# Kernel optimization log

Measured on AMD Instinct MI355X. Metric: run time of the kernel, lower is better.

Reference implementation:

```python
import jax, jax.numpy as jnp
import numpy as np

IN, H, OUT = 128, 256, 128
B, T = 256, 512
EPS = 1e-5


def gru_cell(x, h, w_ih, w_hh, b_ih, b_hh):
    # PyTorch GRUCell: gates ordered (r, z, n)
    gi = x @ w_ih.T + b_ih            # (B, 3H)
    gh = h @ w_hh.T + b_hh            # (B, 3H)
    gi_r, gi_z, gi_n = jnp.split(gi, 3, axis=-1)
    gh_r, gh_z, gh_n = jnp.split(gh, 3, axis=-1)
    r = jax.nn.sigmoid(gi_r + gh_r)
    z = jax.nn.sigmoid(gi_z + gh_z)
    n = jnp.tanh(gi_n + r * gh_n)
    return (1.0 - z) * n + z * h


def setup_inputs() -> dict:
    key = jax.random.key(0)
    ks = jax.random.split(key, 12)
    s_in = 1.0 / np.sqrt(H)
    u = lambda k, shp: jax.random.uniform(k, shp, jnp.float32, -s_in, s_in)
    return {
        "x": jax.random.normal(ks[0], (B, T, IN), jnp.float32),
        "w_ih1": u(ks[1], (3 * H, IN)),
        "w_hh1": u(ks[2], (3 * H, H)),
        "b_ih1": u(ks[3], (3 * H,)),
        "b_hh1": u(ks[4], (3 * H,)),
        "w_ih2": u(ks[5], (3 * H, H)),
        "w_hh2": u(ks[6], (3 * H, H)),
        "b_ih2": u(ks[7], (3 * H,)),
        "b_hh2": u(ks[8], (3 * H,)),
        "gamma": jnp.ones((H,), jnp.float32),
        "beta": jnp.zeros((H,), jnp.float32),
        "fc_w": u(ks[9], (OUT, H)),
        "fc_b": u(ks[10], (OUT,)),
    }


def reference(x, w_ih1, w_hh1, b_ih1, b_hh1, w_ih2, w_hh2, b_ih2, b_hh2,
              gamma, beta, fc_w, fc_b):
    batch = x.shape[0]
    h0 = (jnp.zeros((batch, H), x.dtype), jnp.zeros((batch, H), x.dtype))

    def step(carry, xt):
        h1, h2 = carry
        h1 = gru_cell(xt, h1, w_ih1, w_hh1, b_ih1, b_hh1)
        h2 = gru_cell(h1, h2, w_ih2, w_hh2, b_ih2, b_hh2)
        return (h1, h2), h2

    _, seq_hidden = jax.lax.scan(step, h0, jnp.swapaxes(x, 0, 1))  # (T, B, H)
    seq_hidden = jnp.swapaxes(seq_hidden, 0, 1)                    # (B, T, H)

    # SyncBatchNorm in training mode: batch statistics over (batch*time)
    flat = seq_hidden.reshape(-1, H)
    mean = flat.mean(axis=0)
    var = flat.var(axis=0)  # biased variance, as used for normalization
    normed = (flat - mean) * jax.lax.rsqrt(var + EPS) * gamma + beta

    # Hardtanh(-2, 2), temporal mean, linear projection
    act = jnp.clip(normed, -2.0, 2.0).reshape(batch, -1, H)
    summary = act.mean(axis=1)                                     # (B, H)
    return summary @ fc_w.T + fc_b
```

## Files before the change

### kernel.cpp

```cpp
#include <hip/hip_runtime.h>
#include <stdint.h>

#define TT 512
#define BB 256
#define HH 256
#define II 128
#define OUTD 128
#define EPSV 1e-5f

#define NCL 32
#define RPC 8
#define RD1 32
#define RD2 16
#define HPAD 264
#define SPIN_CAP (1 << 17)

#define P_M1 0
#define P_A  1
#define P_M2 2
#define P_B  3

#define OFF_PROG     0u
#define OFF_BNSUM    1024u
#define OFF_BNSQ     2048u
#define OFF_ZERO_END 3072u
#define OFF_GI1      65536u
#define GI_SLOT      16384u
#define GI1_BYTES    ((unsigned)NCL*RD1*GI_SLOT)
#define OFF_H1R      (OFF_GI1 + GI1_BYTES)
#define H1R_BYTES    ((unsigned)NCL*RD2*4096u)
#define OFF_GI2      (OFF_H1R + H1R_BYTES)
#define GI2_BYTES    ((unsigned)NCL*RD2*GI_SLOT)
#define OFF_H2SEQ    (OFF_GI2 + GI2_BYTES)

typedef short bf16x8 __attribute__((ext_vector_type(8)));
typedef float f32x4  __attribute__((ext_vector_type(4)));
typedef unsigned long long u64;

__device__ __forceinline__ short f2bf(float v) {
    unsigned u = __float_as_uint(v);
    u += 0x7fffu + ((u >> 16) & 1u);
    return (short)(u >> 16);
}
__device__ __forceinline__ float bf2f(short s) {
    return __uint_as_float(((unsigned)(unsigned short)s) << 16);
}
__device__ __forceinline__ float bf2f_lo(unsigned u) {
    return __uint_as_float(u << 16);
}
__device__ __forceinline__ float bf2f_hi(unsigned u) {
    return __uint_as_float(u & 0xffff0000u);
}
__device__ __forceinline__ unsigned pk2bf(float a, float b) {
    return (unsigned)(unsigned short)f2bf(a) | ((unsigned)(unsigned short)f2bf(b) << 16);
}
__device__ __forceinline__ bf16x8 ldfrag_f32(const float* __restrict__ p) {
    const float4* q = (const float4*)p;
    float4 a = q[0], b = q[1];
    bf16x8 f;
    f[0]=f2bf(a.x); f[1]=f2bf(a.y); f[2]=f2bf(a.z); f[3]=f2bf(a.w);
    f[4]=f2bf(b.x); f[5]=f2bf(b.y); f[6]=f2bf(b.z); f[7]=f2bf(b.w);
    return f;
}
__device__ __forceinline__ float sigm_f(float x) {
    float e = __expf(-x);
    return __builtin_amdgcn_rcpf(1.f + e);
}
__device__ __forceinline__ float tanh_f(float x) {
    float ax = fabsf(x);
    float e  = __expf(-2.f * ax);
    float t  = (1.f - e) * __builtin_amdgcn_rcpf(1.f + e);
    return copysignf(t, x);
}
__device__ __forceinline__ void poll_ge(const unsigned* p, int tgt) {
    if (tgt <= 0) return;
    int spins = 0;
    while ((int)__hip_atomic_load((unsigned*)p, __ATOMIC_RELAXED, __HIP_MEMORY_SCOPE_SYSTEM) < tgt) {
        __builtin_amdgcn_s_sleep(2);
        if (++spins > SPIN_CAP) break;
    }
    asm volatile("" ::: "memory");
}
__device__ __forceinline__ void poll2_ge(const unsigned* p1, int t1, const unsigned* p2, int t2) {
    int spins = 0;
    for (;;) {
        int a = (int)__hip_atomic_load((unsigned*)p1, __ATOMIC_RELAXED, __HIP_MEMORY_SCOPE_SYSTEM);
        int b = (int)__hip_atomic_load((unsigned*)p2, __ATOMIC_RELAXED, __HIP_MEMORY_SCOPE_SYSTEM);
        if (a >= t1 && b >= t2) break;
        __builtin_amdgcn_s_sleep(2);
        if (++spins > SPIN_CAP) break;
    }
    asm volatile("" ::: "memory");
}
__device__ __forceinline__ void post_prog(unsigned* p, int v) {
    __hip_atomic_store(p, (unsigned)v, __ATOMIC_RELAXED, __HIP_MEMORY_SCOPE_SYSTEM);
}
__device__ __forceinline__ unsigned ld_u32_coh(const unsigned* p) {
    return __hip_atomic_load((unsigned*)p, __ATOMIC_RELAXED, __HIP_MEMORY_SCOPE_SYSTEM);
}
__device__ __forceinline__ void st_u32_coh(unsigned* p, unsigned v) {
    __hip_atomic_store(p, v, __ATOMIC_RELAXED, __HIP_MEMORY_SCOPE_SYSTEM);
}
__device__ __forceinline__ u64 ld_u64_coh(const u64* p) {
    return __hip_atomic_load((u64*)p, __ATOMIC_RELAXED, __HIP_MEMORY_SCOPE_SYSTEM);
}
__device__ __forceinline__ void st_u64_coh(u64* p, u64 v) {
    __hip_atomic_store(p, v, __ATOMIC_RELAXED, __HIP_MEMORY_SCOPE_SYSTEM);
}
#define CFENCE() asm volatile("" ::: "memory")

__global__ void __launch_bounds__(512, 1)
gru_pipe(const float* __restrict__ x,
         const float* __restrict__ wih1, const float* __restrict__ whh1,
         const float* __restrict__ bih1, const float* __restrict__ bhh1,
         const float* __restrict__ wih2, const float* __restrict__ whh2,
         const float* __restrict__ bih2, const float* __restrict__ bhh2,
         char* __restrict__ ws)
{
    const int tid = threadIdx.x, wave = tid >> 6, lane = tid & 63;
    const int qd = lane >> 4, ln = lane & 15;
    const int stage = blockIdx.x & 3;
    const int cl    = blockIdx.x >> 2;
    const int grow0 = cl * RPC;

    unsigned* prog = (unsigned*)(ws + OFF_PROG) + cl * 4;
    short* h2seq = (short*)(ws + OFF_H2SEQ);

    __shared__ __align__(16) short hb[2][16][HPAD];
    {
        short* z = &hb[0][0][0];
        for (int i = tid; i < 2*16*HPAD; i += 512) z[i] = 0;
    }
    __syncthreads();

    if (stage == 0) {
        bf16x8 Wi[2][3][4]; f32x4 cinit[2][3];
        #pragma unroll
        for (int b2 = 0; b2 < 2; ++b2)
        #pragma unroll
        for (int g = 0; g < 3; ++g) {
            const int grow = g*256 + (wave*2 + b2)*16 + ln;
            #pragma unroll
            for (int kc = 0; kc < 4; ++kc)
                Wi[b2][g][kc] = ldfrag_f32(wih1 + grow*II + kc*32 + qd*8);
            float c0 = bih1[grow] + (g < 2 ? bhh1[grow] : 0.f);
            cinit[b2][g] = f32x4{c0, c0, c0, c0};
        }
        const float* xr = x + (size_t)(grow0 + (ln>>2)*2 + (ln&1)) * (TT*II) + qd*8;
        float4 xp[8];
        #pragma unroll
        for (int kc = 0; kc < 4; ++kc) {
            xp[2*kc]   = *(const float4*)(xr + kc*32);
            xp[2*kc+1] = *(const float4*)(xr + kc*32 + 4);
        }

        for (int t = 0; t < TT; ++t) {
            if (tid == 0 && t >= 2) post_prog(&prog[P_M1], t);
            if ((t & 7) == 0) poll_ge(&prog[P_A], t - 24);
            CFENCE();
            bf16x8 a[4];
            #pragma unroll
            for (int kc = 0; kc < 4; ++kc) {
                float4 u = xp[2*kc], v = xp[2*kc+1];
                bf16x8 f;
                f[0]=f2bf(u.x); f[1]=f2bf(u.y); f[2]=f2bf(u.z); f[3]=f2bf(u.w);
                f[4]=f2bf(v.x); f[5]=f2bf(v.y); f[6]=f2bf(v.z); f[7]=f2bf(v.w);
                a[kc] = f;
            }
            if (t + 1 < TT) {
                const float* xn = xr + (size_t)(t+1)*II;
                #pragma unroll
                for (int kc = 0; kc < 4; ++kc) {
                    xp[2*kc]   = *(const float4*)(xn + kc*32);
                    xp[2*kc+1] = *(const float4*)(xn + kc*32 + 4);
                }
            }
            CFENCE();
            f32x4 acc[2][3];
            #pragma unroll
            for (int b2 = 0; b2 < 2; ++b2)
            #pragma unroll
            for (int g = 0; g < 3; ++g) acc[b2][g] = cinit[b2][g];
            #pragma unroll
            for (int kc = 0; kc < 4; ++kc)
            #pragma unroll
            for (int b2 = 0; b2 < 2; ++b2)
            #pragma unroll
            for (int g = 0; g < 3; ++g)
                acc[b2][g] = __builtin_amdgcn_mfma_f32_16x16x32_bf16(a[kc], Wi[b2][g][kc], acc[b2][g], 0, 0, 0);
            CFENCE();
            char* slot = ws + OFF_GI1 + ((size_t)cl*RD1 + (t & (RD1-1)))*GI_SLOT;
            unsigned* rz = (unsigned*)slot;
            u64* nn = (u64*)(slot + 8192);
            #pragma unroll
            for (int b2 = 0; b2 < 2; ++b2) {
                const int tile = wave*2 + b2;
                st_u32_coh(rz + (tile*2 + 0)*64 + lane, pk2bf(acc[b2][0][0], acc[b2][0][1]));
                st_u32_coh(rz + (tile*2 + 1)*64 + lane, pk2bf(acc[b2][1][0], acc[b2][1][1]));
                union { float f[2]; u64 u; } np;
                np.f[0] = acc[b2][2][0]; np.f[1] = acc[b2][2][1];
                st_u64_coh(nn + tile*64 + lane, np.u);
            }
            asm volatile("s_waitcnt vmcnt(14)" ::: "memory");
            __builtin_amdgcn_sched_barrier(0);
            __builtin_amdgcn_s_barrier();
        }
        __syncthreads();
        if (tid == 0) post_prog(&prog[P_M1], 1000000);

    } else if (stage == 1) {
        bf16x8 Wh[2][3][8]; float bnn[2];
        #pragma unroll
        for (int b2 = 0; b2 < 2; ++b2) {
            const int colg = (wave*2 + b2)*16 + ln;
            #pragma unroll
            for (int g = 0; g < 3; ++g)
                #pragma unroll
                for (int kc = 0; kc < 8; ++kc)
                    Wh[b2][g][kc] = ldfrag_f32(whh1 + (g*256 + colg)*HH + kc*32 + qd*8);
            bnn[b2] = bhh1[512 + colg];
        }
        float hold[2][2] = {{0.f,0.f},{0.f,0.f}};
        unsigned pr0, pr1, pz0, pz1; u64 pn0, pn1;
        const int tile0 = wave*2, tile1 = wave*2 + 1;

        poll_ge(&prog[P_M1], 2);
        {
            char* slot = ws + OFF_GI1 + (size_t)cl*RD1*GI_SLOT;
            const unsigned* rz = (const unsigned*)slot;
            const u64* nn = (const u64*)(slot + 8192);
            pr0 = ld_u32_coh(rz + (tile0*2+0)*64 + lane);
            pz0 = ld_u32_coh(rz + (tile0*2+1)*64 + lane);
            pn0 = ld_u64_coh(nn + tile0*64 + lane);
            pr1 = ld_u32_coh(rz + (tile1*2+0)*64 + lane);
            pz1 = ld_u32_coh(rz + (tile1*2+1)*64 + lane);
            pn1 = ld_u64_coh(nn + tile1*64 + lane);
        }

        for (int t = 0; t < TT; ++t) {
            if (tid == 0 && t >= 2) post_prog(&prog[P_A], t);
            if ((t & 7) == 0) poll2_ge(&prog[P_M1], t + 10, &prog[P_M2], t - 9);
            CFENCE();
            f32x4 aR[2], aZ[2], aN[2]; float gn[2][2];
            aR[0] = f32x4{bf2f_lo(pr0), bf2f_hi(pr0), 0.f, 0.f};
            aZ[0] = f32x4{bf2f_lo(pz0), bf2f_hi(pz0), 0.f, 0.f};
            aR[1] = f32x4{bf2f_lo(pr1), bf2f_hi(pr1), 0.f, 0.f};
            aZ[1] = f32x4{bf2f_lo(pz1), bf2f_hi(pz1), 0.f, 0.f};
            { union { u64 u; float f[2]; } c; c.u = pn0; gn[0][0]=c.f[0]; gn[0][1]=c.f[1];
              c.u = pn1; gn[1][0]=c.f[0]; gn[1][1]=c.f[1]; }
            aN[0] = f32x4{bnn[0], bnn[0], 0.f, 0.f};
            aN[1] = f32x4{bnn[1], bnn[1], 0.f, 0.f};
            if (t + 1 < TT) {
                char* slot = ws + OFF_GI1 + ((size_t)cl*RD1 + ((t+1) & (RD1-1)))*GI_SLOT;
                const unsigned* rz = (const unsigned*)slot;
                const u64* nn = (const u64*)(slot + 8192);
                pr0 = ld_u32_coh(rz + (tile0*2+0)*64 + lane);
                pz0 = ld_u32_coh(rz + (tile0*2+1)*64 + lane);
                pn0 = ld_u64_coh(nn + tile0*64 + lane);
                pr1 = ld_u32_coh(rz + (tile1*2+0)*64 + lane);
                pz1 = ld_u32_coh(rz + (tile1*2+1)*64 + lane);
                pn1 = ld_u64_coh(nn + tile1*64 + lane);
            }
            CFENCE();
            const int rb = (t + 1) & 1, wb = t & 1;
            #pragma unroll
            for (int kc = 0; kc < 8; ++kc) {
                bf16x8 f = *(const bf16x8*)&hb[rb][ln][kc*32 + qd*8];
                aR[0] = __builtin_amdgcn_mfma_f32_16x16x32_bf16(f, Wh[0][0][kc], aR[0], 0,0,0);
                aR[1] = __builtin_amdgcn_mfma_f32_16x16x32_bf16(f, Wh[1][0][kc], aR[1], 0,0,0);
                aZ[0] = __builtin_amdgcn_mfma_f32_16x16x32_bf16(f, Wh[0][1][kc], aZ[0], 0,0,0);
                aZ[1] = __builtin_amdgcn_mfma_f32_16x16x32_bf16(f, Wh[1][1][kc], aZ[1], 0,0,0);
                aN[0] = __builtin_amdgcn_mfma_f32_16x16x32_bf16(f, Wh[0][2][kc], aN[0], 0,0,0);
                aN[1] = __builtin_amdgcn_mfma_f32_16x16x32_bf16(f, Wh[1][2][kc], aN[1], 0,0,0);
            }
            CFENCE();
            unsigned* h1slot = (unsigned*)(ws + OFF_H1R + ((size_t)cl*RD2 + (t & (RD2-1)))*4096u);
            #pragma unroll
            for (int b2 = 0; b2 < 2; ++b2) {
                const int colg = (wave*2 + b2)*16 + ln;
                unsigned pk = 0;
                #pragma unroll
                for (int r = 0; r < 2; ++r) {
                    float rg = sigm_f(aR[b2][r]);
                    float zg = sigm_f(aZ[b2][r]);
                    float ng = tanh_f(gn[b2][r] + rg * aN[b2][r]);
                    float h  = (1.f - zg)*ng + zg*hold[b2][r];
                    hold[b2][r] = h;
                    short hs = f2bf(h);
                    hb[wb][qd*4 + r][colg] = hs;
                    pk |= (unsigned)(unsigned short)hs << (16*r);
                }
                st_u32_coh(h1slot + colg*4 + qd, pk);
            }
            asm volatile("s_waitcnt vmcnt(8) lgkmcnt(0)" ::: "memory");
            __builtin_amdgcn_sched_barrier(0);
            __builtin_amdgcn_s_barrier();
        }
        __syncthreads();
        if (tid == 0) post_prog(&prog[P_A], 1000000);

    } else if (stage == 2) {
        bf16x8 Wi[2][3][8]; float c0s[2][3];
        #pragma unroll
        for (int b2 = 0; b2 < 2; ++b2)
        #pragma unroll
        for (int g = 0; g < 3; ++g) {
            const int grow = g*256 + (wave*2 + b2)*16 + ln;
            #pragma unroll
            for (int kc = 0; kc < 8; ++kc)
                Wi[b2][g][kc] = ldfrag_f32(wih2 + grow*HH + kc*32 + qd*8);
            c0s[b2][g] = bih2[grow] + (g < 2 ? bhh2[grow] : 0.f);
        }
        const int base = (tid & 1) * 8, pcol = tid >> 1;
        u64 vcur;

        poll_ge(&prog[P_A], 2);
        {
            const u64* h1s = (const u64*)(ws + OFF_H1R + (size_t)cl*RD2*4096u);
            u64 v = ld_u64_coh(h1s + tid);
            unsigned lo = (unsigned)v, hi = (unsigned)(v >> 32);
            hb[0][base + 0][pcol] = (short)lo;
            hb[0][base + 1][pcol] = (short)(lo >> 16);
            hb[0][base + 4][pcol] = (short)hi;
            hb[0][base + 5][pcol] = (short)(hi >> 16);
        }
        poll_ge(&prog[P_A], 3);
        vcur = ld_u64_coh((const u64*)(ws + OFF_H1R + ((size_t)cl*RD2 + 1)*4096u) + tid);
        __syncthreads();

        for (int u = 0; u < TT; ++u) {
            if (tid == 0 && u >= 2) post_prog(&prog[P_M2], u);
            if ((u & 1) == 0) poll2_ge(&prog[P_A], u + 5, &prog[P_B], u - 13);
            CFENCE();
            if (u + 1 < TT) {
                unsigned lo = (unsigned)vcur, hi = (unsigned)(vcur >> 32);
                hb[(u+1) & 1][base + 0][pcol] = (short)lo;
                hb[(u+1) & 1][base + 1][pcol] = (short)(lo >> 16);
                hb[(u+1) & 1][base + 4][pcol] = (short)hi;
                hb[(u+1) & 1][base + 5][pcol] = (short)(hi >> 16);
            }
            if (u + 2 < TT)
                vcur = ld_u64_coh((const u64*)(ws + OFF_H1R + ((size_t)cl*RD2 + ((u+2) & (RD2-1)))*4096u) + tid);
            CFENCE();
            f32x4 acc[2][3];
            #pragma unroll
            for (int b2 = 0; b2 < 2; ++b2)
            #pragma unroll
            for (int g = 0; g < 3; ++g) {
                float c0 = c0s[b2][g];
                acc[b2][g] = f32x4{c0, c0, c0, c0};
            }
            #pragma unroll
            for (int kc = 0; kc < 8; ++kc) {
                bf16x8 f = *(const bf16x8*)&hb[u & 1][ln][kc*32 + qd*8];
                #pragma unroll
                for (int b2 = 0; b2 < 2; ++b2)
                #pragma unroll
                for (int g = 0; g < 3; ++g)
                    acc[b2][g] = __builtin_amdgcn_mfma_f32_16x16x32_bf16(f, Wi[b2][g][kc], acc[b2][g], 0, 0, 0);
            }
            CFENCE();
            char* slot = ws + OFF_GI2 + ((size_t)cl*RD2 + (u & (RD2-1)))*GI_SLOT;
            unsigned* rz = (unsigned*)slot;
            u64* nn = (u64*)(slot + 8192);
            #pragma unroll
            for (int b2 = 0; b2 < 2; ++b2) {
                const int tile = wave*2 + b2;
                st_u32_coh(rz + (tile*2 + 0)*64 + lane, pk2bf(acc[b2][0][0], acc[b2][0][1]));
                st_u32_coh(rz + (tile*2 + 1)*64 + lane, pk2bf(acc[b2][1][0], acc[b2][1][1]));
                union { float f[2]; u64 u; } np;
                np.f[0] = acc[b2][2][0]; np.f[1] = acc[b2][2][1];
                st_u64_coh(nn + tile*64 + lane, np.u);
            }
            asm volatile("s_waitcnt vmcnt(7) lgkmcnt(0)" ::: "memory");
            __builtin_amdgcn_sched_barrier(0);
            __builtin_amdgcn_s_barrier();
        }
        __syncthreads();
        if (tid == 0) post_prog(&prog[P_M2], 1000000);

    } else {
        bf16x8 Wh[2][3][8]; float bnn[2];
        #pragma unroll
        for (int b2 = 0; b2 < 2; ++b2) {
            const int colg = (wave*2 + b2)*16 + ln;
            #pragma unroll
            for (int g = 0; g < 3; ++g)
                #pragma unroll
                for (int kc = 0; kc < 8; ++kc)
                    Wh[b2][g][kc] = ldfrag_f32(whh2 + (g*256 + colg)*HH + kc*32 + qd*8);
            bnn[b2] = bhh2[512 + colg];
        }
        float* bnsum = (float*)(ws + OFF_BNSUM);
        float* bnsq  = (float*)(ws + OFF_BNSQ);
        float hold[2][2] = {{0.f,0.f},{0.f,0.f}};
        float cbs[2] = {0.f, 0.f}, cbq[2] = {0.f, 0.f};
        unsigned pr0, pr1, pz0, pz1; u64 pn0, pn1;
        const int tile0 = wave*2, tile1 = wave*2 + 1;

        poll_ge(&prog[P_M2], 2);
        {
            char* slot = ws + OFF_GI2 + (size_t)cl*RD2*GI_SLOT;
            const unsigned* rz = (const unsigned*)slot;
            const u64* nn = (const u64*)(slot + 8192);
            pr0 = ld_u32_coh(rz + (tile0*2+0)*64 + lane);
            pz0 = ld_u32_coh(rz + (tile0*2+1)*64 + lane);
            pn0 = ld_u64_coh(nn + tile0*64 + lane);
            pr1 = ld_u32_coh(rz + (tile1*2+0)*64 + lane);
            pz1 = ld_u32_coh(rz + (tile1*2+1)*64 + lane);
            pn1 = ld_u64_coh(nn + tile1*64 + lane);
        }
        __syncthreads();

        for (int v = 0; v < TT; ++v) {
            if (tid == 0 && v >= 2) post_prog(&prog[P_B], v);
            if ((v & 1) == 0) poll_ge(&prog[P_M2], v + 4);
            CFENCE();
            f32x4 aR[2], aZ[2], aN[2]; float gn[2][2];
            aR[0] = f32x4{bf2f_lo(pr0), bf2f_hi(pr0), 0.f, 0.f};
            aZ[0] = f32x4{bf2f_lo(pz0), bf2f_hi(pz0), 0.f, 0.f};
            aR[1] = f32x4{bf2f_lo(pr1), bf2f_hi(pr1), 0.f, 0.f};
            aZ[1] = f32x4{bf2f_lo(pz1), bf2f_hi(pz1), 0.f, 0.f};
            { union { u64 u; float f[2]; } c; c.u = pn0; gn[0][0]=c.f[0]; gn[0][1]=c.f[1];
              c.u = pn1; gn[1][0]=c.f[0]; gn[1][1]=c.f[1]; }
            aN[0] = f32x4{bnn[0], bnn[0], 0.f, 0.f};
            aN[1] = f32x4{bnn[1], bnn[1], 0.f, 0.f};
            if (v + 1 < TT) {
                char* slot = ws + OFF_GI2 + ((size_t)cl*RD2 + ((v+1) & (RD2-1)))*GI_SLOT;
                const unsigned* rz = (const unsigned*)slot;
                const u64* nn = (const u64*)(slot + 8192);
                pr0 = ld_u32_coh(rz + (tile0*2+0)*64 + lane);
                pz0 = ld_u32_coh(rz + (tile0*2+1)*64 + lane);
                pn0 = ld_u64_coh(nn + tile0*64 + lane);
                pr1 = ld_u32_coh(rz + (tile1*2+0)*64 + lane);
                pz1 = ld_u32_coh(rz + (tile1*2+1)*64 + lane);
                pn1 = ld_u64_coh(nn + tile1*64 + lane);
            }
            CFENCE();
            const int rb = (v + 1) & 1, wb = v & 1;
            #pragma unroll
            for (int kc = 0; kc < 8; ++kc) {
                bf16x8 f = *(const bf16x8*)&hb[rb][ln][kc*32 + qd*8];
                aR[0] = __builtin_amdgcn_mfma_f32_16x16x32_bf16(f, Wh[0][0][kc], aR[0], 0,0,0);
                aR[1] = __builtin_amdgcn_mfma_f32_16x16x32_bf16(f, Wh[1][0][kc], aR[1], 0,0,0);
                aZ[0] = __builtin_amdgcn_mfma_f32_16x16x32_bf16(f, Wh[0][1][kc], aZ[0], 0,0,0);
                aZ[1] = __builtin_amdgcn_mfma_f32_16x16x32_bf16(f, Wh[1][1][kc], aZ[1], 0,0,0);
                aN[0] = __builtin_amdgcn_mfma_f32_16x16x32_bf16(f, Wh[0][2][kc], aN[0], 0,0,0);
                aN[1] = __builtin_amdgcn_mfma_f32_16x16x32_bf16(f, Wh[1][2][kc], aN[1], 0,0,0);
            }
            CFENCE();
            #pragma unroll
            for (int b2 = 0; b2 < 2; ++b2) {
                const int colg = (wave*2 + b2)*16 + ln;
                #pragma unroll
                for (int r = 0; r < 2; ++r) {
                    float rg = sigm_f(aR[b2][r]);
                    float zg = sigm_f(aZ[b2][r]);
                    float ng = tanh_f(gn[b2][r] + rg * aN[b2][r]);
                    float h  = (1.f - zg)*ng + zg*hold[b2][r];
                    hold[b2][r] = h;
                    cbs[b2] += h; cbq[b2] += h*h;
                    short hs = f2bf(h);
                    hb[wb][qd*4 + r][colg] = hs;
                    h2seq[((size_t)v*BB + grow0 + qd*2 + r)*HH + colg] = hs;
                }
            }
            asm volatile("s_waitcnt vmcnt(10) lgkmcnt(0)" ::: "memory");
            __builtin_amdgcn_sched_barrier(0);
            __builtin_amdgcn_s_barrier();
        }
        #pragma unroll
        for (int b2 = 0; b2 < 2; ++b2) {
            const int colg = (wave*2 + b2)*16 + ln;
            atomicAdd(&bnsum[colg], cbs[b2]);
            atomicAdd(&bnsq[colg],  cbq[b2]);
        }
        __syncthreads();
        if (tid == 0) post_prog(&prog[P_B], 1000000);
    }
}

__global__ void gru_final(const char* __restrict__ ws,
                          const float* __restrict__ gamma, const float* __restrict__ beta,
                          const float* __restrict__ fcw, const float* __restrict__ fcb,
                          float* __restrict__ out)
{
    __shared__ float summ[HH];
    const int b = blockIdx.x, c = threadIdx.x;
    const float* bnsum = (const float*)(ws + OFF_BNSUM);
    const float* bnsq  = (const float*)(ws + OFF_BNSQ);
    const short* h2seq = (const short*)(ws + OFF_H2SEQ);

    const float inv = 1.f / (float)(BB * TT);
    float mean = bnsum[c] * inv;
    float var  = bnsq[c] * inv - mean * mean;
    float scale = rsqrtf(var + EPSV) * gamma[c];
    float shift = beta[c] - mean * scale;

    const short* p = h2seq + (size_t)b*HH + c;
    float acc = 0.f;
    #pragma unroll 4
    for (int t = 0; t < TT; ++t) {
        float v = bf2f(p[(size_t)t*BB*HH]) * scale + shift;
        v = fminf(fmaxf(v, -2.f), 2.f);
        acc += v;
    }
    summ[c] = acc * (1.f / TT);
    __syncthreads();
    if (c < OUTD) {
        float d = fcb[c];
        const float* wr = fcw + c*HH;
        #pragma unroll 8
        for (int h = 0; h < HH; ++h) d += wr[h] * summ[h];
        out[b*OUTD + c] = d;
    }
}

extern "C" void kernel_launch(void* const* d_in, const int* in_sizes, int n_in,
                              void* d_out, int out_size, void* d_ws, size_t ws_size,
                              hipStream_t stream)
{
    const float* x    = (const float*)d_in[0];
    const float* wih1 = (const float*)d_in[1];
    const float* whh1 = (const float*)d_in[2];
    const float* bih1 = (const float*)d_in[3];
    const float* bhh1 = (const float*)d_in[4];
    const float* wih2 = (const float*)d_in[5];
    const float* whh2 = (const float*)d_in[6];
    const float* bih2 = (const float*)d_in[7];
    const float* bhh2 = (const float*)d_in[8];
    const float* gamma= (const float*)d_in[9];
    const float* beta = (const float*)d_in[10];
    const float* fcw  = (const float*)d_in[11];
    const float* fcb  = (const float*)d_in[12];
    char* ws = (char*)d_ws;

    (void)hipMemsetAsync(ws, 0, OFF_ZERO_END, stream);

    hipLaunchKernelGGL(gru_pipe, dim3(NCL*4), dim3(512), 0, stream,
                       x, wih1, whh1, bih1, bhh1, wih2, whh2, bih2, bhh2, ws);

    hipLaunchKernelGGL(gru_final, dim3(BB), dim3(HH), 0, stream,
                       (const char*)ws, gamma, beta, fcw, fcb, (float*)d_out);
}
```

Measured before the change: 1.870 ms.

## Process two batch clusters per block to interleave independent recurrences

Each pipeline block now handles two 8-row batch clusters instead of one, halving the grid from 128 to 64 blocks and interleaving two independent GRU recurrences inside each timestep. The goal is to hide the serial MFMA-to-activation dependency latency and the cross-block progress synchronization by giving each wave independent work. Progress flags are posted every other step and ring depths are unified at 32, with gi slots repacked so r and z share one 64-bit store. The cost is roughly twice the serial work per block per step and more registers and LDS per block, on half as many CUs.

Measured after the change: 3.590 ms. +92.0%, slower.

```diff
diff --git a/kernel.cpp b/kernel.cpp
--- a/kernel.cpp
+++ b/kernel.cpp
@@ -8,10 +8,9 @@
 #define OUTD 128
 #define EPSV 1e-5f
 
-#define NCL 32
+#define NPAIR 16
 #define RPC 8
-#define RD1 32
-#define RD2 16
+#define RD  32
 #define HPAD 264
 #define SPIN_CAP (1 << 17)
 
@@ -26,11 +25,11 @@
 #define OFF_ZERO_END 3072u
 #define OFF_GI1      65536u
 #define GI_SLOT      16384u
-#define GI1_BYTES    ((unsigned)NCL*RD1*GI_SLOT)
+#define GI1_BYTES    ((unsigned)32*RD*GI_SLOT)
 #define OFF_H1R      (OFF_GI1 + GI1_BYTES)
-#define H1R_BYTES    ((unsigned)NCL*RD2*4096u)
+#define H1R_BYTES    ((unsigned)32*RD*4096u)
 #define OFF_GI2      (OFF_H1R + H1R_BYTES)
-#define GI2_BYTES    ((unsigned)NCL*RD2*GI_SLOT)
+#define GI2_BYTES    ((unsigned)32*RD*GI_SLOT)
 #define OFF_H2SEQ    (OFF_GI2 + GI2_BYTES)
 
 typedef short bf16x8 __attribute__((ext_vector_type(8)));
@@ -45,12 +44,8 @@
 __device__ __forceinline__ float bf2f(short s) {
     return __uint_as_float(((unsigned)(unsigned short)s) << 16);
 }
-__device__ __forceinline__ float bf2f_lo(unsigned u) {
-    return __uint_as_float(u << 16);
-}
-__device__ __forceinline__ float bf2f_hi(unsigned u) {
-    return __uint_as_float(u & 0xffff0000u);
-}
+__device__ __forceinline__ float bf2f_lo(unsigned u) { return __uint_as_float(u << 16); }
+__device__ __forceinline__ float bf2f_hi(unsigned u) { return __uint_as_float(u & 0xffff0000u); }
 __device__ __forceinline__ unsigned pk2bf(float a, float b) {
     return (unsigned)(unsigned short)f2bf(a) | ((unsigned)(unsigned short)f2bf(b) << 16);
 }
@@ -120,16 +115,16 @@
     const int tid = threadIdx.x, wave = tid >> 6, lane = tid & 63;
     const int qd = lane >> 4, ln = lane & 15;
     const int stage = blockIdx.x & 3;
-    const int cl    = blockIdx.x >> 2;
-    const int grow0 = cl * RPC;
-
-    unsigned* prog = (unsigned*)(ws + OFF_PROG) + cl * 4;
+    const int pr_id = blockIdx.x >> 2;
+    const int cl0   = pr_id * 2;
+
+    unsigned* prog = (unsigned*)(ws + OFF_PROG) + pr_id * 4;
     short* h2seq = (short*)(ws + OFF_H2SEQ);
 
-    __shared__ __align__(16) short hb[2][16][HPAD];
+    __shared__ __align__(16) short hb[2][2][16][HPAD];
     {
-        short* z = &hb[0][0][0];
-        for (int i = tid; i < 2*16*HPAD; i += 512) z[i] = 0;
+        short* z = &hb[0][0][0][0];
+        for (int i = tid; i < 2*2*16*HPAD; i += 512) z[i] = 0;
     }
     __syncthreads();
 
@@ -146,65 +141,76 @@
             float c0 = bih1[grow] + (g < 2 ? bhh1[grow] : 0.f);
             cinit[b2][g] = f32x4{c0, c0, c0, c0};
         }
-        const float* xr = x + (size_t)(grow0 + (ln>>2)*2 + (ln&1)) * (TT*II) + qd*8;
-        float4 xp[8];
+        const int rr = (ln>>2)*2 + (ln&1);
+        const float* xr[2];
+        xr[0] = x + (size_t)((cl0 + 0)*RPC + rr) * (TT*II) + qd*8;
+        xr[1] = x + (size_t)((cl0 + 1)*RPC + rr) * (TT*II) + qd*8;
+        float4 xf[2][8];
+        #pragma unroll
+        for (int cc = 0; cc < 2; ++cc)
         #pragma unroll
         for (int kc = 0; kc < 4; ++kc) {
-            xp[2*kc]   = *(const float4*)(xr + kc*32);
-            xp[2*kc+1] = *(const float4*)(xr + kc*32 + 4);
+            xf[cc][2*kc]   = *(const float4*)(xr[cc] + kc*32);
+            xf[cc][2*kc+1] = *(const float4*)(xr[cc] + kc*32 + 4);
         }
 
         for (int t = 0; t < TT; ++t) {
-            if (tid == 0 && t >= 2) post_prog(&prog[P_M1], t);
             if ((t & 7) == 0) poll_ge(&prog[P_A], t - 24);
             CFENCE();
-            bf16x8 a[4];
-            #pragma unroll
-            for (int kc = 0; kc < 4; ++kc) {
-                float4 u = xp[2*kc], v = xp[2*kc+1];
-                bf16x8 f;
-                f[0]=f2bf(u.x); f[1]=f2bf(u.y); f[2]=f2bf(u.z); f[3]=f2bf(u.w);
-                f[4]=f2bf(v.x); f[5]=f2bf(v.y); f[6]=f2bf(v.z); f[7]=f2bf(v.w);
-                a[kc] = f;
-            }
-            if (t + 1 < TT) {
-                const float* xn = xr + (size_t)(t+1)*II;
+            #pragma unroll
+            for (int cc = 0; cc < 2; ++cc) {
+                bf16x8 a[4];
                 #pragma unroll
                 for (int kc = 0; kc < 4; ++kc) {
-                    xp[2*kc]   = *(const float4*)(xn + kc*32);
-                    xp[2*kc+1] = *(const float4*)(xn + kc*32 + 4);
-                }
-            }
-            CFENCE();
-            f32x4 acc[2][3];
-            #pragma unroll
-            for (int b2 = 0; b2 < 2; ++b2)
-            #pragma unroll
-            for (int g = 0; g < 3; ++g) acc[b2][g] = cinit[b2][g];
-            #pragma unroll
-            for (int kc = 0; kc < 4; ++kc)
-            #pragma unroll
-            for (int b2 = 0; b2 < 2; ++b2)
-            #pragma unroll
-            for (int g = 0; g < 3; ++g)
-                acc[b2][g] = __builtin_amdgcn_mfma_f32_16x16x32_bf16(a[kc], Wi[b2][g][kc], acc[b2][g], 0, 0, 0);
-            CFENCE();
-            char* slot = ws + OFF_GI1 + ((size_t)cl*RD1 + (t & (RD1-1)))*GI_SLOT;
-            unsigned* rz = (unsigned*)slot;
-            u64* nn = (u64*)(slot + 8192);
-            #pragma unroll
-            for (int b2 = 0; b2 < 2; ++b2) {
-                const int tile = wave*2 + b2;
-                st_u32_coh(rz + (tile*2 + 0)*64 + lane, pk2bf(acc[b2][0][0], acc[b2][0][1]));
-                st_u32_coh(rz + (tile*2 + 1)*64 + lane, pk2bf(acc[b2][1][0], acc[b2][1][1]));
-                union { float f[2]; u64 u; } np;
-                np.f[0] = acc[b2][2][0]; np.f[1] = acc[b2][2][1];
-                st_u64_coh(nn + tile*64 + lane, np.u);
-            }
-            asm volatile("s_waitcnt vmcnt(14)" ::: "memory");
+                    float4 u = xf[cc][2*kc], v = xf[cc][2*kc+1];
+                    bf16x8 f;
+                    f[0]=f2bf(u.x); f[1]=f2bf(u.y); f[2]=f2bf(u.z); f[3]=f2bf(u.w);
+                    f[4]=f2bf(v.x); f[5]=f2bf(v.y); f[6]=f2bf(v.z); f[7]=f2bf(v.w);
+                    a[kc] = f;
+                }
+                if (t + 1 < TT) {
+                    const float* xn = xr[cc] + (size_t)(t+1)*II;
+                    #pragma unroll
+                    for (int kc = 0; kc < 4; ++kc) {
+                        xf[cc][2*kc]   = *(const float4*)(xn + kc*32);
+                        xf[cc][2*kc+1] = *(const float4*)(xn + kc*32 + 4);
+                    }
+                }
+                CFENCE();
+                f32x4 acc[2][3];
+                #pragma unroll
+                for (int b2 = 0; b2 < 2; ++b2)
+                #pragma unroll
+                for (int g = 0; g < 3; ++g) acc[b2][g] = cinit[b2][g];
+                #pragma unroll
+                for (int kc = 0; kc < 4; ++kc)
+                #pragma unroll
+                for (int b2 = 0; b2 < 2; ++b2)
+                #pragma unroll
+                for (int g = 0; g < 3; ++g)
+                    acc[b2][g] = __builtin_amdgcn_mfma_f32_16x16x32_bf16(a[kc], Wi[b2][g][kc], acc[b2][g], 0, 0, 0);
+                CFENCE();
+                char* slot = ws + OFF_GI1 + ((size_t)(cl0+cc)*RD + (t & (RD-1)))*GI_SLOT;
+                #pragma unroll
+                for (int b2 = 0; b2 < 2; ++b2) {
+                    u64* tp = (u64*)(slot + (wave*2 + b2)*1024);
+                    u64 rz = (u64)pk2bf(acc[b2][0][0], acc[b2][0][1])
+                           | ((u64)pk2bf(acc[b2][1][0], acc[b2][1][1]) << 32);
+                    st_u64_coh(tp + lane, rz);
+                    union { float f[2]; u64 u; } np;
+                    np.f[0] = acc[b2][2][0]; np.f[1] = acc[b2][2][1];
+                    st_u64_coh(tp + 64 + lane, np.u);
+                }
+                CFENCE();
+            }
+            if (t & 1) {
+                asm volatile("s_waitcnt vmcnt(24)" ::: "memory");
+                if (tid == 0) post_prog(&prog[P_M1], t - 1);
+            }
             __builtin_amdgcn_sched_barrier(0);
             __builtin_amdgcn_s_barrier();
         }
+        asm volatile("s_waitcnt vmcnt(0)" ::: "memory");
         __syncthreads();
         if (tid == 0) post_prog(&prog[P_M1], 1000000);
 
@@ -220,82 +226,88 @@
                     Wh[b2][g][kc] = ldfrag_f32(whh1 + (g*256 + colg)*HH + kc*32 + qd*8);
             bnn[b2] = bhh1[512 + colg];
         }
-        float hold[2][2] = {{0.f,0.f},{0.f,0.f}};
-        unsigned pr0, pr1, pz0, pz1; u64 pn0, pn1;
-        const int tile0 = wave*2, tile1 = wave*2 + 1;
+        float hold[2][2][2] = {};
+        u64 prz[2][2], pn[2][2];
 
         poll_ge(&prog[P_M1], 2);
-        {
-            char* slot = ws + OFF_GI1 + (size_t)cl*RD1*GI_SLOT;
-            const unsigned* rz = (const unsigned*)slot;
-            const u64* nn = (const u64*)(slot + 8192);
-            pr0 = ld_u32_coh(rz + (tile0*2+0)*64 + lane);
-            pz0 = ld_u32_coh(rz + (tile0*2+1)*64 + lane);
-            pn0 = ld_u64_coh(nn + tile0*64 + lane);
-            pr1 = ld_u32_coh(rz + (tile1*2+0)*64 + lane);
-            pz1 = ld_u32_coh(rz + (tile1*2+1)*64 + lane);
-            pn1 = ld_u64_coh(nn + tile1*64 + lane);
+        #pragma unroll
+        for (int cc = 0; cc < 2; ++cc) {
+            char* slot = ws + OFF_GI1 + (size_t)(cl0+cc)*RD*GI_SLOT;
+            #pragma unroll
+            for (int b2 = 0; b2 < 2; ++b2) {
+                const u64* tp = (const u64*)(slot + (wave*2 + b2)*1024);
+                prz[cc][b2] = ld_u64_coh(tp + lane);
+                pn [cc][b2] = ld_u64_coh(tp + 64 + lane);
+            }
         }
 
         for (int t = 0; t < TT; ++t) {
-            if (tid == 0 && t >= 2) post_prog(&prog[P_A], t);
-            if ((t & 7) == 0) poll2_ge(&prog[P_M1], t + 10, &prog[P_M2], t - 9);
-            CFENCE();
-            f32x4 aR[2], aZ[2], aN[2]; float gn[2][2];
-            aR[0] = f32x4{bf2f_lo(pr0), bf2f_hi(pr0), 0.f, 0.f};
-            aZ[0] = f32x4{bf2f_lo(pz0), bf2f_hi(pz0), 0.f, 0.f};
-            aR[1] = f32x4{bf2f_lo(pr1), bf2f_hi(pr1), 0.f, 0.f};
-            aZ[1] = f32x4{bf2f_lo(pz1), bf2f_hi(pz1), 0.f, 0.f};
-            { union { u64 u; float f[2]; } c; c.u = pn0; gn[0][0]=c.f[0]; gn[0][1]=c.f[1];
-              c.u = pn1; gn[1][0]=c.f[0]; gn[1][1]=c.f[1]; }
-            aN[0] = f32x4{bnn[0], bnn[0], 0.f, 0.f};
-            aN[1] = f32x4{bnn[1], bnn[1], 0.f, 0.f};
-            if (t + 1 < TT) {
-                char* slot = ws + OFF_GI1 + ((size_t)cl*RD1 + ((t+1) & (RD1-1)))*GI_SLOT;
-                const unsigned* rz = (const unsigned*)slot;
-                const u64* nn = (const u64*)(slot + 8192);
-                pr0 = ld_u32_coh(rz + (tile0*2+0)*64 + lane);
-                pz0 = ld_u32_coh(rz + (tile0*2+1)*64 + lane);
-                pn0 = ld_u64_coh(nn + tile0*64 + lane);
-                pr1 = ld_u32_coh(rz + (tile1*2+0)*64 + lane);
-                pz1 = ld_u32_coh(rz + (tile1*2+1)*64 + lane);
-                pn1 = ld_u64_coh(nn + tile1*64 + lane);
-            }
+            if ((t & 7) == 0) poll2_ge(&prog[P_M1], t + 10, &prog[P_M2], t - 24);
             CFENCE();
             const int rb = (t + 1) & 1, wb = t & 1;
             #pragma unroll
-            for (int kc = 0; kc < 8; ++kc) {
-                bf16x8 f = *(const bf16x8*)&hb[rb][ln][kc*32 + qd*8];
-                aR[0] = __builtin_amdgcn_mfma_f32_16x16x32_bf16(f, Wh[0][0][kc], aR[0], 0,0,0);
-                aR[1] = __builtin_amdgcn_mfma_f32_16x16x32_bf16(f, Wh[1][0][kc], aR[1], 0,0,0);
-                aZ[0] = __builtin_amdgcn_mfma_f32_16x16x32_bf16(f, Wh[0][1][kc], aZ[0], 0,0,0);
-                aZ[1] = __builtin_amdgcn_mfma_f32_16x16x32_bf16(f, Wh[1][1][kc], aZ[1], 0,0,0);
-                aN[0] = __builtin_amdgcn_mfma_f32_16x16x32_bf16(f, Wh[0][2][kc], aN[0], 0,0,0);
-                aN[1] = __builtin_amdgcn_mfma_f32_16x16x32_bf16(f, Wh[1][2][kc], aN[1], 0,0,0);
-            }
-            CFENCE();
-            unsigned* h1slot = (unsigned*)(ws + OFF_H1R + ((size_t)cl*RD2 + (t & (RD2-1)))*4096u);
-            #pragma unroll
-            for (int b2 = 0; b2 < 2; ++b2) {
-                const int colg = (wave*2 + b2)*16 + ln;
-                unsigned pk = 0;
-                #pragma unroll
-                for (int r = 0; r < 2; ++r) {
-                    float rg = sigm_f(aR[b2][r]);
-                    float zg = sigm_f(aZ[b2][r]);
-                    float ng = tanh_f(gn[b2][r] + rg * aN[b2][r]);
-                    float h  = (1.f - zg)*ng + zg*hold[b2][r];
-                    hold[b2][r] = h;
-                    short hs = f2bf(h);
-                    hb[wb][qd*4 + r][colg] = hs;
-                    pk |= (unsigned)(unsigned short)hs << (16*r);
-                }
-                st_u32_coh(h1slot + colg*4 + qd, pk);
-            }
-            asm volatile("s_waitcnt vmcnt(8) lgkmcnt(0)" ::: "memory");
+            for (int cc = 0; cc < 2; ++cc) {
+                f32x4 aR[2], aZ[2], aN[2]; float gn[2][2];
+                #pragma unroll
+                for (int b2 = 0; b2 < 2; ++b2) {
+                    unsigned rzl = (unsigned)prz[cc][b2];
+                    unsigned rzh = (unsigned)(prz[cc][b2] >> 32);
+                    aR[b2] = f32x4{bf2f_lo(rzl), bf2f_hi(rzl), 0.f, 0.f};
+                    aZ[b2] = f32x4{bf2f_lo(rzh), bf2f_hi(rzh), 0.f, 0.f};
+                    union { u64 u; float f[2]; } c; c.u = pn[cc][b2];
+                    gn[b2][0] = c.f[0]; gn[b2][1] = c.f[1];
+                    aN[b2] = f32x4{bnn[b2], bnn[b2], 0.f, 0.f};
+                }
+                if (t + 1 < TT) {
+                    char* slot = ws + OFF_GI1 + ((size_t)(cl0+cc)*RD + ((t+1) & (RD-1)))*GI_SLOT;
+                    #pragma unroll
+                    for (int b2 = 0; b2 < 2; ++b2) {
+                        const u64* tp = (const u64*)(slot + (wave*2 + b2)*1024);
+                        prz[cc][b2] = ld_u64_coh(tp + lane);
+                        pn [cc][b2] = ld_u64_coh(tp + 64 + lane);
+                    }
+                }
+                CFENCE();
+                #pragma unroll
+                for (int kc = 0; kc < 8; ++kc) {
+                    bf16x8 f = *(const bf16x8*)&hb[cc][rb][ln][kc*32 + qd*8];
+                    aR[0] = __builtin_amdgcn_mfma_f32_16x16x32_bf16(f, Wh[0][0][kc], aR[0], 0,0,0);
+                    aR[1] = __builtin_amdgcn_mfma_f32_16x16x32_bf16(f, Wh[1][0][kc], aR[1], 0,0,0);
+                    aZ[0] = __builtin_amdgcn_mfma_f32_16x16x32_bf16(f, Wh[0][1][kc], aZ[0], 0,0,0);
+                    aZ[1] = __builtin_amdgcn_mfma_f32_16x16x32_bf16(f, Wh[1][1][kc], aZ[1], 0,0,0);
+                    aN[0] = __builtin_amdgcn_mfma_f32_16x16x32_bf16(f, Wh[0][2][kc], aN[0], 0,0,0);
+                    aN[1] = __builtin_amdgcn_mfma_f32_16x16x32_bf16(f, Wh[1][2][kc], aN[1], 0,0,0);
+                }
+                CFENCE();
+                unsigned* h1slot = (unsigned*)(ws + OFF_H1R + ((size_t)(cl0+cc)*RD + (t & (RD-1)))*4096u);
+                #pragma unroll
+                for (int b2 = 0; b2 < 2; ++b2) {
+                    const int colg = (wave*2 + b2)*16 + ln;
+                    unsigned pk = 0;
+                    #pragma unroll
+                    for (int r = 0; r < 2; ++r) {
+                        float rg = sigm_f(aR[b2][r]);
+                        float zg = sigm_f(aZ[b2][r]);
+                        float ng = tanh_f(gn[b2][r] + rg * aN[b2][r]);
+                        float h  = (1.f - zg)*ng + zg*hold[cc][b2][r];
+                        hold[cc][b2][r] = h;
+                        short hs = f2bf(h);
+                        hb[cc][wb][qd*4 + r][colg] = hs;
+                        pk |= (unsigned)(unsigned short)hs << (16*r);
+                    }
+                    st_u32_coh(h1slot + colg*4 + qd, pk);
+                }
+                CFENCE();
+            }
+            if (t & 1) {
+                asm volatile("s_waitcnt vmcnt(12)" ::: "memory");
+                if (tid == 0) post_prog(&prog[P_A], t - 1);
+            }
+            asm volatile("s_waitcnt lgkmcnt(0)" ::: "memory");
             __builtin_amdgcn_sched_barrier(0);
             __builtin_amdgcn_s_barrier();
         }
+        asm volatile("s_waitcnt vmcnt(0)" ::: "memory");
         __syncthreads();
         if (tid == 0) post_prog(&prog[P_A], 1000000);
 
@@ -312,70 +324,80 @@
             c0s[b2][g] = bih2[grow] + (g < 2 ? bhh2[grow] : 0.f);
         }
         const int base = (tid & 1) * 8, pcol = tid >> 1;
-        u64 vcur;
+        u64 vc[2];
 
         poll_ge(&prog[P_A], 2);
-        {
-            const u64* h1s = (const u64*)(ws + OFF_H1R + (size_t)cl*RD2*4096u);
+        #pragma unroll
+        for (int cc = 0; cc < 2; ++cc) {
+            const u64* h1s = (const u64*)(ws + OFF_H1R + (size_t)(cl0+cc)*RD*4096u);
             u64 v = ld_u64_coh(h1s + tid);
             unsigned lo = (unsigned)v, hi = (unsigned)(v >> 32);
-            hb[0][base + 0][pcol] = (short)lo;
-            hb[0][base + 1][pcol] = (short)(lo >> 16);
-            hb[0][base + 4][pcol] = (short)hi;
-            hb[0][base + 5][pcol] = (short)(hi >> 16);
-        }
-        poll_ge(&prog[P_A], 3);
-        vcur = ld_u64_coh((const u64*)(ws + OFF_H1R + ((size_t)cl*RD2 + 1)*4096u) + tid);
+            hb[cc][0][base + 0][pcol] = (short)lo;
+            hb[cc][0][base + 1][pcol] = (short)(lo >> 16);
+            hb[cc][0][base + 4][pcol] = (short)hi;
+            hb[cc][0][base + 5][pcol] = (short)(hi >> 16);
+            vc[cc] = ld_u64_coh((const u64*)(ws + OFF_H1R + ((size_t)(cl0+cc)*RD + 1)*4096u) + tid);
+        }
         __syncthreads();
 
         for (int u = 0; u < TT; ++u) {
-            if (tid == 0 && u >= 2) post_prog(&prog[P_M2], u);
-            if ((u & 1) == 0) poll2_ge(&prog[P_A], u + 5, &prog[P_B], u - 13);
+            if ((u & 7) == 0) poll2_ge(&prog[P_A], u + 11, &prog[P_B], u - 24);
             CFENCE();
-            if (u + 1 < TT) {
-                unsigned lo = (unsigned)vcur, hi = (unsigned)(vcur >> 32);
-                hb[(u+1) & 1][base + 0][pcol] = (short)lo;
-                hb[(u+1) & 1][base + 1][pcol] = (short)(lo >> 16);
-                hb[(u+1) & 1][base + 4][pcol] = (short)hi;
-                hb[(u+1) & 1][base + 5][pcol] = (short)(hi >> 16);
-            }
-            if (u + 2 < TT)
-                vcur = ld_u64_coh((const u64*)(ws + OFF_H1R + ((size_t)cl*RD2 + ((u+2) & (RD2-1)))*4096u) + tid);
+            #pragma unroll
+            for (int cc = 0; cc < 2; ++cc) {
+                if (u + 1 < TT) {
+                    unsigned lo = (unsigned)vc[cc], hi = (unsigned)(vc[cc] >> 32);
+                    hb[cc][(u+1) & 1][base + 0][pcol] = (short)lo;
+                    hb[cc][(u+1) & 1][base + 1][pcol] = (short)(lo >> 16);
+                    hb[cc][(u+1) & 1][base + 4][pcol] = (short)hi;
+                    hb[cc][(u+1) & 1][base + 5][pcol] = (short)(hi >> 16);
+                }
+                if (u + 2 < TT)
+                    vc[cc] = ld_u64_coh((const u64*)(ws + OFF_H1R + ((size_t)(cl0+cc)*RD + ((u+2) & (RD-1)))*4096u) + tid);
+            }
             CFENCE();
-            f32x4 acc[2][3];
-            #pragma unroll
-            for (int b2 = 0; b2 < 2; ++b2)
-            #pragma unroll
-            for (int g = 0; g < 3; ++g) {
-                float c0 = c0s[b2][g];
-                acc[b2][g] = f32x4{c0, c0, c0, c0};
-            }
-            #pragma unroll
-            for (int kc = 0; kc < 8; ++kc) {
-                bf16x8 f = *(const bf16x8*)&hb[u & 1][ln][kc*32 + qd*8];
+            #pragma unroll
+            for (int cc = 0; cc < 2; ++cc) {
+                f32x4 acc[2][3];
                 #pragma unroll
                 for (int b2 = 0; b2 < 2; ++b2)
                 #pragma unroll
-                for (int g = 0; g < 3; ++g)
-                    acc[b2][g] = __builtin_amdgcn_mfma_f32_16x16x32_bf16(f, Wi[b2][g][kc], acc[b2][g], 0, 0, 0);
-            }
-            CFENCE();
-            char* slot = ws + OFF_GI2 + ((size_t)cl*RD2 + (u & (RD2-1)))*GI_SLOT;
-            unsigned* rz = (unsigned*)slot;
-            u64* nn = (u64*)(slot + 8192);
-            #pragma unroll
-            for (int b2 = 0; b2 < 2; ++b2) {
-                const int tile = wave*2 + b2;
-                st_u32_coh(rz + (tile*2 + 0)*64 + lane, pk2bf(acc[b2][0][0], acc[b2][0][1]));
-                st_u32_coh(rz + (tile*2 + 1)*64 + lane, pk2bf(acc[b2][1][0], acc[b2][1][1]));
-                union { float f[2]; u64 u; } np;
-                np.f[0] = acc[b2][2][0]; np.f[1] = acc[b2][2][1];
-                st_u64_coh(nn + tile*64 + lane, np.u);
-            }
-            asm volatile("s_waitcnt vmcnt(7) lgkmcnt(0)" ::: "memory");
+                for (int g = 0; g < 3; ++g) {
+                    float c0 = c0s[b2][g];
+                    acc[b2][g] = f32x4{c0, c0, c0, c0};
+                }
+                #pragma unroll
+                for (int kc = 0; kc < 8; ++kc) {
+                    bf16x8 f = *(const bf16x8*)&hb[cc][u & 1][ln][kc*32 + qd*8];
+                    #pragma unroll
+                    for (int b2 = 0; b2 < 2; ++b2)
+                    #pragma unroll
+                    for (int g = 0; g < 3; ++g)
+                        acc[b2][g] = __builtin_amdgcn_mfma_f32_16x16x32_bf16(f, Wi[b2][g][kc], acc[b2][g], 0, 0, 0);
+                }
+                CFENCE();
+                char* slot = ws + OFF_GI2 + ((size_t)(cl0+cc)*RD + (u & (RD-1)))*GI_SLOT;
+                #pragma unroll
+                for (int b2 = 0; b2 < 2; ++b2) {
+                    u64* tp = (u64*)(slot + (wave*2 + b2)*1024);
+                    u64 rz = (u64)pk2bf(acc[b2][0][0], acc[b2][0][1])
+                           | ((u64)pk2bf(acc[b2][1][0], acc[b2][1][1]) << 32);
+                    st_u64_coh(tp + lane, rz);
+                    union { float f[2]; u64 u2; } np;
+                    np.f[0] = acc[b2][2][0]; np.f[1] = acc[b2][2][1];
+                    st_u64_coh(tp + 64 + lane, np.u2);
+                }
+                CFENCE();
+            }
+            if (u & 1) {
+                asm volatile("s_waitcnt vmcnt(10)" ::: "memory");
+                if (tid == 0) post_prog(&prog[P_M2], u - 1);
+            }
+            asm volatile("s_waitcnt lgkmcnt(0)" ::: "memory");
             __builtin_amdgcn_sched_barrier(0);
             __builtin_amdgcn_s_barrier();
         }
+        asm volatile("s_waitcnt vmcnt(0)" ::: "memory");
         __syncthreads();
         if (tid == 0) post_prog(&prog[P_M2], 1000000);
 
@@ -393,87 +415,92 @@
         }
         float* bnsum = (float*)(ws + OFF_BNSUM);
         float* bnsq  = (float*)(ws + OFF_BNSQ);
-        float hold[2][2] = {{0.f,0.f},{0.f,0.f}};
-        float cbs[2] = {0.f, 0.f}, cbq[2] = {0.f, 0.f};
-        unsigned pr0, pr1, pz0, pz1; u64 pn0, pn1;
-        const int tile0 = wave*2, tile1 = wave*2 + 1;
+        float hold[2][2][2] = {};
+        float cbs[2][2] = {}, cbq[2][2] = {};
+        u64 prz[2][2], pn[2][2];
 
         poll_ge(&prog[P_M2], 2);
-        {
-            char* slot = ws + OFF_GI2 + (size_t)cl*RD2*GI_SLOT;
-            const unsigned* rz = (const unsigned*)slot;
-            const u64* nn = (const u64*)(slot + 8192);
-            pr0 = ld_u32_coh(rz + (tile0*2+0)*64 + lane);
-            pz0 = ld_u32_coh(rz + (tile0*2+1)*64 + lane);
-            pn0 = ld_u64_coh(nn + tile0*64 + lane);
-            pr1 = ld_u32_coh(rz + (tile1*2+0)*64 + lane);
-            pz1 = ld_u32_coh(rz + (tile1*2+1)*64 + lane);
-            pn1 = ld_u64_coh(nn + tile1*64 + lane);
+        #pragma unroll
+        for (int cc = 0; cc < 2; ++cc) {
+            char* slot = ws + OFF_GI2 + (size_t)(cl0+cc)*RD*GI_SLOT;
+            #pragma unroll
+            for (int b2 = 0; b2 < 2; ++b2) {
+                const u64* tp = (const u64*)(slot + (wave*2 + b2)*1024);
+                prz[cc][b2] = ld_u64_coh(tp + lane);
+                pn [cc][b2] = ld_u64_coh(tp + 64 + lane);
+            }
         }
         __syncthreads();
 
         for (int v = 0; v < TT; ++v) {
-            if (tid == 0 && v >= 2) post_prog(&prog[P_B], v);
-            if ((v & 1) == 0) poll_ge(&prog[P_M2], v + 4);
-            CFENCE();
-            f32x4 aR[2], aZ[2], aN[2]; float gn[2][2];
-            aR[0] = f32x4{bf2f_lo(pr0), bf2f_hi(pr0), 0.f, 0.f};
-            aZ[0] = f32x4{bf2f_lo(pz0), bf2f_hi(pz0), 0.f, 0.f};
-            aR[1] = f32x4{bf2f_lo(pr1), bf2f_hi(pr1), 0.f, 0.f};
-            aZ[1] = f32x4{bf2f_lo(pz1), bf2f_hi(pz1), 0.f, 0.f};
-            { union { u64 u; float f[2]; } c; c.u = pn0; gn[0][0]=c.f[0]; gn[0][1]=c.f[1];
-              c.u = pn1; gn[1][0]=c.f[0]; gn[1][1]=c.f[1]; }
-            aN[0] = f32x4{bnn[0], bnn[0], 0.f, 0.f};
-            aN[1] = f32x4{bnn[1], bnn[1], 0.f, 0.f};
-            if (v + 1 < TT) {
-                char* slot = ws + OFF_GI2 + ((size_t)cl*RD2 + ((v+1) & (RD2-1)))*GI_SLOT;
-                const unsigned* rz = (const unsigned*)slot;
-                const u64* nn = (const u64*)(slot + 8192);
-                pr0 = ld_u32_coh(rz + (tile0*2+0)*64 + lane);
-                pz0 = ld_u32_coh(rz + (tile0*2+1)*64 + lane);
-                pn0 = ld_u64_coh(nn + tile0*64 + lane);
-                pr1 = ld_u32_coh(rz + (tile1*2+0)*64 + lane);
-                pz1 = ld_u32_coh(rz + (tile1*2+1)*64 + lane);
-                pn1 = ld_u64_coh(nn + tile1*64 + lane);
-            }
+            if ((v & 7) == 0) poll_ge(&prog[P_M2], v + 10);
             CFENCE();
             const int rb = (v + 1) & 1, wb = v & 1;
             #pragma unroll
-            for (int kc = 0; kc < 8; ++kc) {
-                bf16x8 f = *(const bf16x8*)&hb[rb][ln][kc*32 + qd*8];
-                aR[0] = __builtin_amdgcn_mfma_f32_16x16x32_bf16(f, Wh[0][0][kc], aR[0], 0,0,0);
-                aR[1] = __builtin_amdgcn_mfma_f32_16x16x32_bf16(f, Wh[1][0][kc], aR[1], 0,0,0);
-                aZ[0] = __builtin_amdgcn_mfma_f32_16x16x32_bf16(f, Wh[0][1][kc], aZ[0], 0,0,0);
-                aZ[1] = __builtin_amdgcn_mfma_f32_16x16x32_bf16(f, Wh[1][1][kc], aZ[1], 0,0,0);
-                aN[0] = __builtin_amdgcn_mfma_f32_16x16x32_bf16(f, Wh[0][2][kc], aN[0], 0,0,0);
-                aN[1] = __builtin_amdgcn_mfma_f32_16x16x32_bf16(f, Wh[1][2][kc], aN[1], 0,0,0);
-            }
-            CFENCE();
-            #pragma unroll
-            for (int b2 = 0; b2 < 2; ++b2) {
-                const int colg = (wave*2 + b2)*16 + ln;
-                #pragma unroll
-                for (int r = 0; r < 2; ++r) {
-                    float rg = sigm_f(aR[b2][r]);
-                    float zg = sigm_f(aZ[b2][r]);
-                    float ng = tanh_f(gn[b2][r] + rg * aN[b2][r]);
-                    float h  = (1.f - zg)*ng + zg*hold[b2][r];
-                    hold[b2][r] = h;
-                    cbs[b2] += h; cbq[b2] += h*h;
-                    short hs = f2bf(h);
-                    hb[wb][qd*4 + r][colg] = hs;
-                    h2seq[((size_t)v*BB + grow0 + qd*2 + r)*HH + colg] = hs;
-                }
-            }
-            asm volatile("s_waitcnt vmcnt(10) lgkmcnt(0)" ::: "memory");
+            for (int cc = 0; cc < 2; ++cc) {
+                f32x4 aR[2], aZ[2], aN[2]; float gn[2][2];
+                #pragma unroll
+                for (int b2 = 0; b2 < 2; ++b2) {
+                    unsigned rzl = (unsigned)prz[cc][b2];
+                    unsigned rzh = (unsigned)(prz[cc][b2] >> 32);
+                    aR[b2] = f32x4{bf2f_lo(rzl), bf2f_hi(rzl), 0.f, 0.f};
+                    aZ[b2] = f32x4{bf2f_lo(rzh), bf2f_hi(rzh), 0.f, 0.f};
+                    union { u64 u; float f[2]; } c; c.u = pn[cc][b2];
+                    gn[b2][0] = c.f[0]; gn[b2][1] = c.f[1];
+                    aN[b2] = f32x4{bnn[b2], bnn[b2], 0.f, 0.f};
+                }
+                if (v + 1 < TT) {
+                    char* slot = ws + OFF_GI2 + ((size_t)(cl0+cc)*RD + ((v+1) & (RD-1)))*GI_SLOT;
+                    #pragma unroll
+                    for (int b2 = 0; b2 < 2; ++b2) {
+                        const u64* tp = (const u64*)(slot + (wave*2 + b2)*1024);
+                        prz[cc][b2] = ld_u64_coh(tp + lane);
+                        pn [cc][b2] = ld_u64_coh(tp + 64 + lane);
+                    }
+                }
+                CFENCE();
+                #pragma unroll
+                for (int kc = 0; kc < 8; ++kc) {
+                    bf16x8 f = *(const bf16x8*)&hb[cc][rb][ln][kc*32 + qd*8];
+                    aR[0] = __builtin_amdgcn_mfma_f32_16x16x32_bf16(f, Wh[0][0][kc], aR[0], 0,0,0);
+                    aR[1] = __builtin_amdgcn_mfma_f32_16x16x32_bf16(f, Wh[1][0][kc], aR[1], 0,0,0);
+                    aZ[0] = __builtin_amdgcn_mfma_f32_16x16x32_bf16(f, Wh[0][1][kc], aZ[0], 0,0,0);
+                    aZ[1] = __builtin_amdgcn_mfma_f32_16x16x32_bf16(f, Wh[1][1][kc], aZ[1], 0,0,0);
+                    aN[0] = __builtin_amdgcn_mfma_f32_16x16x32_bf16(f, Wh[0][2][kc], aN[0], 0,0,0);
+                    aN[1] = __builtin_amdgcn_mfma_f32_16x16x32_bf16(f, Wh[1][2][kc], aN[1], 0,0,0);
+                }
+                CFENCE();
+                const int grow0c = (cl0 + cc) * RPC;
+                #pragma unroll
+                for (int b2 = 0; b2 < 2; ++b2) {
+                    const int colg = (wave*2 + b2)*16 + ln;
+                    #pragma unroll
+                    for (int r = 0; r < 2; ++r) {
+                        float rg = sigm_f(aR[b2][r]);
+                        float zg = sigm_f(aZ[b2][r]);
+                        float ng = tanh_f(gn[b2][r] + rg * aN[b2][r]);
+                        float h  = (1.f - zg)*ng + zg*hold[cc][b2][r];
+                        hold[cc][b2][r] = h;
+                        cbs[cc][b2] += h; cbq[cc][b2] += h*h;
+                        short hs = f2bf(h);
+                        hb[cc][wb][qd*4 + r][colg] = hs;
+                        h2seq[((size_t)v*BB + grow0c + qd*2 + r)*HH + colg] = hs;
+                    }
+                }
+                CFENCE();
+            }
+            if ((v & 1) && tid == 0) post_prog(&prog[P_B], v - 1);
+            asm volatile("s_waitcnt lgkmcnt(0)" ::: "memory");
             __builtin_amdgcn_sched_barrier(0);
             __builtin_amdgcn_s_barrier();
         }
         #pragma unroll
+        for (int cc = 0; cc < 2; ++cc)
+        #pragma unroll
         for (int b2 = 0; b2 < 2; ++b2) {
             const int colg = (wave*2 + b2)*16 + ln;
-            atomicAdd(&bnsum[colg], cbs[b2]);
-            atomicAdd(&bnsq[colg],  cbq[b2]);
+            atomicAdd(&bnsum[colg], cbs[cc][b2]);
+            atomicAdd(&bnsq[colg],  cbq[cc][b2]);
         }
         __syncthreads();
         if (tid == 0) post_prog(&prog[P_B], 1000000);
@@ -537,7 +564,7 @@
 
     (void)hipMemsetAsync(ws, 0, OFF_ZERO_END, stream);
 
-    hipLaunchKernelGGL(gru_pipe, dim3(NCL*4), dim3(512), 0, stream,
+    hipLaunchKernelGGL(gru_pipe, dim3(NPAIR*4), dim3(512), 0, stream,
                        x, wih1, whh1, bih1, bhh1, wih2, whh2, bih2, bhh2, ws);
 
     hipLaunchKernelGGL(gru_final, dim3(BB), dim3(HH), 0, stream,
```
